# Optimization experiments

Hardware: AMD Instinct MI355X
Metric: run time of the kernel (lower is better)

## Reference

```python
import jax, jax.numpy as jnp
import numpy as np
import math

HEAD_DIM = 64
EMBED_DIM = 512
B, T = 16, 2048

def setup_inputs() -> dict:
    key = jax.random.key(0)
    k1, k2, k3 = jax.random.split(key, 3)
    x = jax.random.normal(k1, (B, T, EMBED_DIM), dtype=jnp.float32)
    # nn.Linear-style init scale
    s = 1.0 / math.sqrt(EMBED_DIM)
    Wq = jax.random.uniform(k2, (EMBED_DIM, HEAD_DIM), dtype=jnp.float32, minval=-s, maxval=s)
    bq = jax.random.uniform(k3, (HEAD_DIM,), dtype=jnp.float32, minval=-s, maxval=s)
    return {"x": x, "Wq": Wq, "bq": bq}

def reference(x, Wq, bq):
    # Faithful to source: q, k, v all come from the SAME query projection.
    q = jnp.einsum('bte,ed->btd', x, Wq) + bq  # [B,T,D]
    d_k = q.shape[-1]
    # weights[b, i, j] = q_i . q_j / sqrt(d_k)
    weights = jnp.einsum('bid,bjd->bij', q, q) / jnp.sqrt(jnp.float32(d_k))
    # NOTE: source applies softmax over dim=1 (query/row axis), not dim=-1.
    weights = jax.nn.softmax(weights, axis=1)
    attention = jnp.einsum('bij,bjd->bid', weights, q)  # v == q in source
    return attention
```

## Files before the change

### kernel.cpp

```cpp
#include <hip/hip_runtime.h>
#include <hip/hip_bf16.h>

#define BN 16
#define TN 2048
#define DN 64
#define EN 512
#define PAD 68

using f32x4  = __attribute__((ext_vector_type(4))) float;
using bf16x8 = __attribute__((ext_vector_type(8))) short;
using bf16x4 = __attribute__((ext_vector_type(4))) short;

static __device__ __forceinline__ short f2bf(float f) {
    __hip_bfloat16 h = __float2bfloat16(f);
    return __builtin_bit_cast(short, h);
}
static __device__ __forceinline__ float bf2f(short s) {
    return __bfloat162float(__builtin_bit_cast(__hip_bfloat16, s));
}

__global__ __launch_bounds__(256) void wprep_kernel(
    const float* __restrict__ Wq, short* __restrict__ WTh,
    short* __restrict__ WTl)
{
    __shared__ float wlds[64][65];
    const int tid = threadIdx.x;
    const int k0 = blockIdx.x * 64;
    #pragma unroll
    for (int it = 0; it < 16; ++it) {
        int idx = it * 256 + tid;
        int k = idx >> 6, n = idx & 63;
        wlds[k][n] = Wq[(size_t)(k0 + k) * 64 + n];
    }
    __syncthreads();
    #pragma unroll
    for (int it = 0; it < 16; ++it) {
        int idx = it * 256 + tid;
        int n = idx >> 6, k = idx & 63;
        float v = wlds[k][n];
        short h = f2bf(v);
        short l = f2bf(v - bf2f(h));
        WTh[(size_t)n * EN + k0 + k] = h;
        WTl[(size_t)n * EN + k0 + k] = l;
    }
}

__global__ __launch_bounds__(256, 2) void qproj_kernel(
    const float* __restrict__ x, const short* __restrict__ WTh,
    const short* __restrict__ WTl, const float* __restrict__ bq,
    short* __restrict__ Qb, short* __restrict__ QTb)
{
    __shared__ short xh[64 * 40];
    __shared__ short wth[64 * 40];
    __shared__ short wtl[64 * 40];
    __shared__ short tl[64][68];

    const int tid = threadIdx.x;
    const int lane = tid & 63;
    const int wv = tid >> 6;
    const int c = lane & 15;
    const int g = lane >> 4;
    const int rowbase = blockIdx.x * 64;
    const int b = rowbase >> 11;
    const int tbase = rowbase & (TN - 1);

    const int sr = tid >> 3;
    const int sc4 = tid & 7;

    float4 xa = *reinterpret_cast<const float4*>(&x[(size_t)(rowbase + sr) * EN + sc4 * 4]);
    float4 xb = *reinterpret_cast<const float4*>(&x[(size_t)(rowbase + 32 + sr) * EN + sc4 * 4]);
    bf16x4 wa = *reinterpret_cast<const bf16x4*>(&WTh[(size_t)sr * EN + sc4 * 4]);
    bf16x4 wb = *reinterpret_cast<const bf16x4*>(&WTh[(size_t)(32 + sr) * EN + sc4 * 4]);
    bf16x4 la = *reinterpret_cast<const bf16x4*>(&WTl[(size_t)sr * EN + sc4 * 4]);
    bf16x4 lb = *reinterpret_cast<const bf16x4*>(&WTl[(size_t)(32 + sr) * EN + sc4 * 4]);

    f32x4 acc[4];
    #pragma unroll
    for (int nt = 0; nt < 4; ++nt) acc[nt] = (f32x4){0.f, 0.f, 0.f, 0.f};

    for (int ks = 0; ks < EN; ks += 32) {
        __syncthreads();
        bf16x4 h0, h1;
        #pragma unroll
        for (int j = 0; j < 4; ++j) { h0[j] = f2bf(xa[j]); h1[j] = f2bf(xb[j]); }
        *reinterpret_cast<bf16x4*>(&xh[sr * 40 + sc4 * 4]) = h0;
        *reinterpret_cast<bf16x4*>(&xh[(32 + sr) * 40 + sc4 * 4]) = h1;
        *reinterpret_cast<bf16x4*>(&wth[sr * 40 + sc4 * 4]) = wa;
        *reinterpret_cast<bf16x4*>(&wth[(32 + sr) * 40 + sc4 * 4]) = wb;
        *reinterpret_cast<bf16x4*>(&wtl[sr * 40 + sc4 * 4]) = la;
        *reinterpret_cast<bf16x4*>(&wtl[(32 + sr) * 40 + sc4 * 4]) = lb;

        const int kn = (ks + 32 < EN) ? ks + 32 : ks;
        xa = *reinterpret_cast<const float4*>(&x[(size_t)(rowbase + sr) * EN + kn + sc4 * 4]);
        xb = *reinterpret_cast<const float4*>(&x[(size_t)(rowbase + 32 + sr) * EN + kn + sc4 * 4]);
        wa = *reinterpret_cast<const bf16x4*>(&WTh[(size_t)sr * EN + kn + sc4 * 4]);
        wb = *reinterpret_cast<const bf16x4*>(&WTh[(size_t)(32 + sr) * EN + kn + sc4 * 4]);
        la = *reinterpret_cast<const bf16x4*>(&WTl[(size_t)sr * EN + kn + sc4 * 4]);
        lb = *reinterpret_cast<const bf16x4*>(&WTl[(size_t)(32 + sr) * EN + kn + sc4 * 4]);
        __syncthreads();

        bf16x8 av = *reinterpret_cast<const bf16x8*>(&xh[(wv * 16 + c) * 40 + g * 8]);
        #pragma unroll
        for (int nt = 0; nt < 4; ++nt) {
            bf16x8 bh = *reinterpret_cast<const bf16x8*>(&wth[(nt * 16 + c) * 40 + g * 8]);
            bf16x8 bl = *reinterpret_cast<const bf16x8*>(&wtl[(nt * 16 + c) * 40 + g * 8]);
            acc[nt] = __builtin_amdgcn_mfma_f32_16x16x32_bf16(av, bh, acc[nt], 0, 0, 0);
            acc[nt] = __builtin_amdgcn_mfma_f32_16x16x32_bf16(av, bl, acc[nt], 0, 0, 0);
        }
    }

    __syncthreads();
    #pragma unroll
    for (int nt = 0; nt < 4; ++nt) {
        const float bias = bq[nt * 16 + c];
        #pragma unroll
        for (int r = 0; r < 4; ++r) {
            const int row = wv * 16 + g * 4 + r;
            short qb = f2bf(acc[nt][r] + bias);
            Qb[(size_t)(rowbase + row) * DN + nt * 16 + c] = qb;
            tl[nt * 16 + c][row] = qb;
        }
    }
    __syncthreads();
    #pragma unroll
    for (int it = 0; it < 4; ++it) {
        int idx = it * 256 + tid;
        int d = idx >> 4;
        int j4 = (idx & 15) * 4;
        *reinterpret_cast<short4*>(&QTb[((size_t)(b * 64 + d)) * TN + tbase + j4]) =
            *reinterpret_cast<const short4*>(&tl[d][j4]);
    }
}

__global__ __launch_bounds__(256, 4) void stats_kernel(
    const short* __restrict__ Qb, float* __restrict__ l_part)
{
    __shared__ short Qt[64 * PAD];
    const int tid = threadIdx.x;
    const int lane = tid & 63;
    const int wv = tid >> 6;
    const int c = lane & 15;
    const int g = lane >> 4;
    const int b = blockIdx.y;
    const int z = blockIdx.z;
    const int jbase = blockIdx.x * 64 + wv * 16;
    const short* Qbb = Qb + (size_t)b * TN * DN;

    bf16x8 a0 = *reinterpret_cast<const bf16x8*>(Qbb + (size_t)(jbase + c) * DN + g * 8);
    bf16x8 a1 = *reinterpret_cast<const bf16x8*>(Qbb + (size_t)(jbase + c) * DN + g * 8 + 32);

    const int srow = tid >> 2;
    const int schk = tid & 3;
    const int ilo = z * (TN / 4);

    bf16x8 v0 = *reinterpret_cast<const bf16x8*>(Qbb + (size_t)(ilo + srow) * DN + schk * 16);
    bf16x8 v1 = *reinterpret_cast<const bf16x8*>(Qbb + (size_t)(ilo + srow) * DN + schk * 16 + 8);

    float l[4] = {0.f, 0.f, 0.f, 0.f};
    for (int ii = 0; ii < TN / 4; ii += 64) {
        __syncthreads();
        *reinterpret_cast<bf16x8*>(&Qt[srow * PAD + schk * 16]) = v0;
        *reinterpret_cast<bf16x8*>(&Qt[srow * PAD + schk * 16 + 8]) = v1;
        const int in_ = ilo + ((ii + 64 < TN / 4) ? ii + 64 : ii);
        v0 = *reinterpret_cast<const bf16x8*>(Qbb + (size_t)(in_ + srow) * DN + schk * 16);
        v1 = *reinterpret_cast<const bf16x8*>(Qbb + (size_t)(in_ + srow) * DN + schk * 16 + 8);
        __syncthreads();

        #pragma unroll
        for (int it = 0; it < 4; ++it) {
            bf16x8 b0 = *reinterpret_cast<const bf16x8*>(&Qt[(it * 16 + c) * PAD + g * 8]);
            bf16x8 b1 = *reinterpret_cast<const bf16x8*>(&Qt[(it * 16 + c) * PAD + g * 8 + 32]);
            f32x4 acc = {0.f, 0.f, 0.f, 0.f};
            acc = __builtin_amdgcn_mfma_f32_16x16x32_bf16(a0, b0, acc, 0, 0, 0);
            acc = __builtin_amdgcn_mfma_f32_16x16x32_bf16(a1, b1, acc, 0, 0, 0);
            #pragma unroll
            for (int r = 0; r < 4; ++r)
                l[r] += __expf(acc[r] * 0.125f);
        }
    }
    #pragma unroll
    for (int r = 0; r < 4; ++r) {
        float v = l[r];
        v += __shfl_xor(v, 1);
        v += __shfl_xor(v, 2);
        v += __shfl_xor(v, 4);
        v += __shfl_xor(v, 8);
        l[r] = v;
    }
    if (c == 0) {
        #pragma unroll
        for (int r = 0; r < 4; ++r)
            l_part[((size_t)z * BN + b) * TN + jbase + g * 4 + r] = l[r];
    }
}

__global__ __launch_bounds__(256) void fuse_kernel(
    const short* __restrict__ QTb, const float* __restrict__ l_part,
    short* __restrict__ RT)
{
    const int idx = blockIdx.x * 256 + threadIdx.x;
    const int c8 = idx & 255;
    const int bd = idx >> 8;
    const int b = bd >> 6;
    const int j0 = c8 * 8;

    bf16x8 q = *reinterpret_cast<const bf16x8*>(&QTb[(size_t)bd * TN + j0]);
    const float* lp0 = l_part + (size_t)b * TN + j0;
    const float* lp1 = l_part + (size_t)(BN + b) * TN + j0;
    const float* lp2 = l_part + (size_t)(2 * BN + b) * TN + j0;
    const float* lp3 = l_part + (size_t)(3 * BN + b) * TN + j0;
    bf16x8 r;
    #pragma unroll
    for (int t = 0; t < 8; ++t)
        r[t] = f2bf(bf2f(q[t]) / (lp0[t] + lp1[t] + lp2[t] + lp3[t]));
    *reinterpret_cast<bf16x8*>(&RT[(size_t)bd * TN + j0]) = r;
}

__global__ __launch_bounds__(256, 2) void pv_kernel(
    const short* __restrict__ Qb, const short* __restrict__ RT,
    float* __restrict__ out0, float* __restrict__ out1)
{
    __shared__ short Qt[64 * PAD];
    __shared__ short RTt[64 * PAD];
    __shared__ short Pt[8][16 * PAD];

    const int tid = threadIdx.x;
    const int lane = tid & 63;
    const int wv = tid >> 6;
    const int c = lane & 15;
    const int g = lane >> 4;
    const int b = blockIdx.y;
    const int z = blockIdx.z;
    const int ibase = blockIdx.x * 128 + wv * 32;
    const short* Qbb = Qb + (size_t)b * TN * DN;
    const short* RTb = RT + (size_t)b * DN * TN;

    bf16x8 bi[2][2];
    #pragma unroll
    for (int ih = 0; ih < 2; ++ih) {
        const short* p = Qbb + (size_t)(ibase + ih * 16 + c) * DN + g * 8;
        bi[ih][0] = *reinterpret_cast<const bf16x8*>(p);
        bi[ih][1] = *reinterpret_cast<const bf16x8*>(p + 32);
    }

    f32x4 o[4][2];
    #pragma unroll
    for (int dt = 0; dt < 4; ++dt)
        #pragma unroll
        for (int ih = 0; ih < 2; ++ih)
            o[dt][ih] = (f32x4){0.f, 0.f, 0.f, 0.f};

    const int srow = tid >> 2;
    const int schk = tid & 3;
    const int jlo = z * (TN / 2);

    bf16x8 vq0 = *reinterpret_cast<const bf16x8*>(Qbb + (size_t)(jlo + srow) * DN + schk * 16);
    bf16x8 vq1 = *reinterpret_cast<const bf16x8*>(Qbb + (size_t)(jlo + srow) * DN + schk * 16 + 8);
    bf16x8 vt0 = *reinterpret_cast<const bf16x8*>(RTb + (size_t)srow * TN + jlo + schk * 16);
    bf16x8 vt1 = *reinterpret_cast<const bf16x8*>(RTb + (size_t)srow * TN + jlo + schk * 16 + 8);

    for (int jj = 0; jj < TN / 2; jj += 64) {
        __syncthreads();
        *reinterpret_cast<bf16x8*>(&Qt[srow * PAD + schk * 16]) = vq0;
        *reinterpret_cast<bf16x8*>(&Qt[srow * PAD + schk * 16 + 8]) = vq1;
        *reinterpret_cast<bf16x8*>(&RTt[srow * PAD + schk * 16]) = vt0;
        *reinterpret_cast<bf16x8*>(&RTt[srow * PAD + schk * 16 + 8]) = vt1;

        const int jn = jlo + ((jj + 64 < TN / 2) ? jj + 64 : jj);
        vq0 = *reinterpret_cast<const bf16x8*>(Qbb + (size_t)(jn + srow) * DN + schk * 16);
        vq1 = *reinterpret_cast<const bf16x8*>(Qbb + (size_t)(jn + srow) * DN + schk * 16 + 8);
        vt0 = *reinterpret_cast<const bf16x8*>(RTb + (size_t)srow * TN + jn + schk * 16);
        vt1 = *reinterpret_cast<const bf16x8*>(RTb + (size_t)srow * TN + jn + schk * 16 + 8);
        __syncthreads();

        bf16x8 aq[4][2];
        #pragma unroll
        for (int dt = 0; dt < 4; ++dt) {
            aq[dt][0] = *reinterpret_cast<const bf16x8*>(&RTt[(dt * 16 + c) * PAD + g * 8]);
            aq[dt][1] = *reinterpret_cast<const bf16x8*>(&RTt[(dt * 16 + c) * PAD + 32 + g * 8]);
        }

        #pragma unroll
        for (int jt = 0; jt < 4; ++jt) {
            bf16x8 a0 = *reinterpret_cast<const bf16x8*>(&Qt[(jt * 16 + c) * PAD + g * 8]);
            bf16x8 a1 = *reinterpret_cast<const bf16x8*>(&Qt[(jt * 16 + c) * PAD + g * 8 + 32]);
            #pragma unroll
            for (int ih = 0; ih < 2; ++ih) {
                f32x4 accs = {0.f, 0.f, 0.f, 0.f};
                accs = __builtin_amdgcn_mfma_f32_16x16x32_bf16(a0, bi[ih][0], accs, 0, 0, 0);
                accs = __builtin_amdgcn_mfma_f32_16x16x32_bf16(a1, bi[ih][1], accs, 0, 0, 0);
                bf16x4 pw;
                #pragma unroll
                for (int r = 0; r < 4; ++r)
                    pw[r] = f2bf(__expf(accs[r] * 0.125f));
                *reinterpret_cast<bf16x4*>(&Pt[wv * 2 + ih][c * PAD + jt * 16 + g * 4]) = pw;
            }
        }
        asm volatile("s_waitcnt lgkmcnt(0)" ::: "memory");
        __builtin_amdgcn_sched_barrier(0);

        #pragma unroll
        for (int ih = 0; ih < 2; ++ih) {
            bf16x8 p0 = *reinterpret_cast<const bf16x8*>(&Pt[wv * 2 + ih][c * PAD + g * 8]);
            bf16x8 p1 = *reinterpret_cast<const bf16x8*>(&Pt[wv * 2 + ih][c * PAD + 32 + g * 8]);
            #pragma unroll
            for (int dt = 0; dt < 4; ++dt) {
                o[dt][ih] = __builtin_amdgcn_mfma_f32_16x16x32_bf16(aq[dt][0], p0, o[dt][ih], 0, 0, 0);
                o[dt][ih] = __builtin_amdgcn_mfma_f32_16x16x32_bf16(aq[dt][1], p1, o[dt][ih], 0, 0, 0);
            }
        }
    }

    float* outb = (z ? out1 : out0) + (size_t)b * TN * DN;
    #pragma unroll
    for (int dt = 0; dt < 4; ++dt) {
        #pragma unroll
        for (int ih = 0; ih < 2; ++ih) {
            float4 v4;
            v4.x = o[dt][ih][0]; v4.y = o[dt][ih][1];
            v4.z = o[dt][ih][2]; v4.w = o[dt][ih][3];
            *reinterpret_cast<float4*>(
                &outb[(size_t)(ibase + ih * 16 + c) * DN + dt * 16 + g * 4]) = v4;
        }
    }
}

__global__ __launch_bounds__(256) void reduce_kernel(
    float* __restrict__ out, const float* __restrict__ part1)
{
    const size_t i = (size_t)blockIdx.x * 256 + threadIdx.x;
    float4 a = reinterpret_cast<float4*>(out)[i];
    float4 b = reinterpret_cast<const float4*>(part1)[i];
    a.x += b.x; a.y += b.y; a.z += b.z; a.w += b.w;
    reinterpret_cast<float4*>(out)[i] = a;
}

extern "C" void kernel_launch(void* const* d_in, const int* in_sizes, int n_in,
                              void* d_out, int out_size, void* d_ws, size_t ws_size,
                              hipStream_t stream) {
    const float* x  = (const float*)d_in[0];
    const float* Wq = (const float*)d_in[1];
    const float* bq = (const float*)d_in[2];
    float* out = (float*)d_out;

    short* Qb   = (short*)d_ws;
    short* QTb  = Qb + (size_t)BN * TN * DN;
    short* RT   = QTb + (size_t)BN * TN * DN;
    float* lpar = (float*)(RT + (size_t)BN * TN * DN);
    short* WTh  = (short*)(lpar + (size_t)4 * BN * TN);
    short* WTl  = WTh + (size_t)DN * EN;
    float* part1 = (float*)(WTl + (size_t)DN * EN);

    wprep_kernel<<<dim3(EN / 64), dim3(256), 0, stream>>>(Wq, WTh, WTl);
    qproj_kernel<<<dim3(BN * TN / 64), dim3(256), 0, stream>>>(x, WTh, WTl, bq, Qb, QTb);
    stats_kernel<<<dim3(TN / 64, BN, 4), dim3(256), 0, stream>>>(Qb, lpar);
    fuse_kernel<<<dim3(BN * DN * TN / 8 / 256), dim3(256), 0, stream>>>(QTb, lpar, RT);
    pv_kernel<<<dim3(TN / 128, BN, 2), dim3(256), 0, stream>>>(Qb, RT, out, part1);
    reduce_kernel<<<dim3(BN * TN * DN / 4 / 256), dim3(256), 0, stream>>>(out, part1);
}
```

Before: 79.22 us.

## Double-buffer LDS tiles in qproj, stats and attention kernels with one barrier

Converts the three tiled kernels from single-buffered LDS staging with two __syncthreads per iteration to ping-pong LDS buffers with a register prefetch two tiles ahead. Each iteration now needs only one lgkmcnt wait plus s_barrier. The aim is to overlap LDS stores of the next tile with MFMA work on the current tile and to halve barrier cost. In exchange LDS use doubles, which may limit occupancy in the attention kernel that also holds Pt.

Result: no change. 78.75 us, median of 2 (-0.6%).

```diff
diff --git a/kernel.cpp b/kernel.cpp
--- a/kernel.cpp
+++ b/kernel.cpp
@@ -17,6 +17,10 @@
 }
 static __device__ __forceinline__ float bf2f(short s) {
     return __bfloat162float(__builtin_bit_cast(__hip_bfloat16, s));
+}
+static __device__ __forceinline__ void bar_lds() {
+    asm volatile("s_waitcnt lgkmcnt(0)" ::: "memory");
+    __builtin_amdgcn_s_barrier();
 }
 
 __global__ __launch_bounds__(256) void wprep_kernel(
@@ -50,9 +54,9 @@
     const short* __restrict__ WTl, const float* __restrict__ bq,
     short* __restrict__ Qb, short* __restrict__ QTb)
 {
-    __shared__ short xh[64 * 40];
-    __shared__ short wth[64 * 40];
-    __shared__ short wtl[64 * 40];
+    __shared__ short xh[2 * 64 * 40];
+    __shared__ short wth[2 * 64 * 40];
+    __shared__ short wtl[2 * 64 * 40];
     __shared__ short tl[64][68];
 
     const int tid = threadIdx.x;
@@ -66,20 +70,21 @@
 
     const int sr = tid >> 3;
     const int sc4 = tid & 7;
-
-    float4 xa = *reinterpret_cast<const float4*>(&x[(size_t)(rowbase + sr) * EN + sc4 * 4]);
-    float4 xb = *reinterpret_cast<const float4*>(&x[(size_t)(rowbase + 32 + sr) * EN + sc4 * 4]);
-    bf16x4 wa = *reinterpret_cast<const bf16x4*>(&WTh[(size_t)sr * EN + sc4 * 4]);
-    bf16x4 wb = *reinterpret_cast<const bf16x4*>(&WTh[(size_t)(32 + sr) * EN + sc4 * 4]);
-    bf16x4 la = *reinterpret_cast<const bf16x4*>(&WTl[(size_t)sr * EN + sc4 * 4]);
-    bf16x4 lb = *reinterpret_cast<const bf16x4*>(&WTl[(size_t)(32 + sr) * EN + sc4 * 4]);
-
-    f32x4 acc[4];
-    #pragma unroll
-    for (int nt = 0; nt < 4; ++nt) acc[nt] = (f32x4){0.f, 0.f, 0.f, 0.f};
-
-    for (int ks = 0; ks < EN; ks += 32) {
-        __syncthreads();
+    const size_t xr0 = (size_t)(rowbase + sr) * EN + sc4 * 4;
+    const size_t xr1 = (size_t)(rowbase + 32 + sr) * EN + sc4 * 4;
+    const size_t wr0 = (size_t)sr * EN + sc4 * 4;
+    const size_t wr1 = (size_t)(32 + sr) * EN + sc4 * 4;
+
+    float4 xa, xb;
+    bf16x4 wa, wb, la, lb;
+
+    xa = *reinterpret_cast<const float4*>(&x[xr0]);
+    xb = *reinterpret_cast<const float4*>(&x[xr1]);
+    wa = *reinterpret_cast<const bf16x4*>(&WTh[wr0]);
+    wb = *reinterpret_cast<const bf16x4*>(&WTh[wr1]);
+    la = *reinterpret_cast<const bf16x4*>(&WTl[wr0]);
+    lb = *reinterpret_cast<const bf16x4*>(&WTl[wr1]);
+    {
         bf16x4 h0, h1;
         #pragma unroll
         for (int j = 0; j < 4; ++j) { h0[j] = f2bf(xa[j]); h1[j] = f2bf(xb[j]); }
@@ -89,24 +94,53 @@
         *reinterpret_cast<bf16x4*>(&wth[(32 + sr) * 40 + sc4 * 4]) = wb;
         *reinterpret_cast<bf16x4*>(&wtl[sr * 40 + sc4 * 4]) = la;
         *reinterpret_cast<bf16x4*>(&wtl[(32 + sr) * 40 + sc4 * 4]) = lb;
-
-        const int kn = (ks + 32 < EN) ? ks + 32 : ks;
-        xa = *reinterpret_cast<const float4*>(&x[(size_t)(rowbase + sr) * EN + kn + sc4 * 4]);
-        xb = *reinterpret_cast<const float4*>(&x[(size_t)(rowbase + 32 + sr) * EN + kn + sc4 * 4]);
-        wa = *reinterpret_cast<const bf16x4*>(&WTh[(size_t)sr * EN + kn + sc4 * 4]);
-        wb = *reinterpret_cast<const bf16x4*>(&WTh[(size_t)(32 + sr) * EN + kn + sc4 * 4]);
-        la = *reinterpret_cast<const bf16x4*>(&WTl[(size_t)sr * EN + kn + sc4 * 4]);
-        lb = *reinterpret_cast<const bf16x4*>(&WTl[(size_t)(32 + sr) * EN + kn + sc4 * 4]);
-        __syncthreads();
-
-        bf16x8 av = *reinterpret_cast<const bf16x8*>(&xh[(wv * 16 + c) * 40 + g * 8]);
+    }
+    xa = *reinterpret_cast<const float4*>(&x[xr0 + 32]);
+    xb = *reinterpret_cast<const float4*>(&x[xr1 + 32]);
+    wa = *reinterpret_cast<const bf16x4*>(&WTh[wr0 + 32]);
+    wb = *reinterpret_cast<const bf16x4*>(&WTh[wr1 + 32]);
+    la = *reinterpret_cast<const bf16x4*>(&WTl[wr0 + 32]);
+    lb = *reinterpret_cast<const bf16x4*>(&WTl[wr1 + 32]);
+    bar_lds();
+
+    f32x4 acc[4];
+    #pragma unroll
+    for (int nt = 0; nt < 4; ++nt) acc[nt] = (f32x4){0.f, 0.f, 0.f, 0.f};
+
+    for (int t = 0; t < 16; ++t) {
+        const int cur = t & 1;
+        const int co = cur * 2560;
+        if (t + 1 < 16) {
+            const int wo = (cur ^ 1) * 2560;
+            bf16x4 h0, h1;
+            #pragma unroll
+            for (int j = 0; j < 4; ++j) { h0[j] = f2bf(xa[j]); h1[j] = f2bf(xb[j]); }
+            *reinterpret_cast<bf16x4*>(&xh[wo + sr * 40 + sc4 * 4]) = h0;
+            *reinterpret_cast<bf16x4*>(&xh[wo + (32 + sr) * 40 + sc4 * 4]) = h1;
+            *reinterpret_cast<bf16x4*>(&wth[wo + sr * 40 + sc4 * 4]) = wa;
+            *reinterpret_cast<bf16x4*>(&wth[wo + (32 + sr) * 40 + sc4 * 4]) = wb;
+            *reinterpret_cast<bf16x4*>(&wtl[wo + sr * 40 + sc4 * 4]) = la;
+            *reinterpret_cast<bf16x4*>(&wtl[wo + (32 + sr) * 40 + sc4 * 4]) = lb;
+        }
+        if (t + 2 < 16) {
+            const int kn = (t + 2) * 32;
+            xa = *reinterpret_cast<const float4*>(&x[xr0 + kn]);
+            xb = *reinterpret_cast<const float4*>(&x[xr1 + kn]);
+            wa = *reinterpret_cast<const bf16x4*>(&WTh[wr0 + kn]);
+            wb = *reinterpret_cast<const bf16x4*>(&WTh[wr1 + kn]);
+            la = *reinterpret_cast<const bf16x4*>(&WTl[wr0 + kn]);
+            lb = *reinterpret_cast<const bf16x4*>(&WTl[wr1 + kn]);
+        }
+
+        bf16x8 av = *reinterpret_cast<const bf16x8*>(&xh[co + (wv * 16 + c) * 40 + g * 8]);
         #pragma unroll
         for (int nt = 0; nt < 4; ++nt) {
-            bf16x8 bh = *reinterpret_cast<const bf16x8*>(&wth[(nt * 16 + c) * 40 + g * 8]);
-            bf16x8 bl = *reinterpret_cast<const bf16x8*>(&wtl[(nt * 16 + c) * 40 + g * 8]);
+            bf16x8 bh = *reinterpret_cast<const bf16x8*>(&wth[co + (nt * 16 + c) * 40 + g * 8]);
+            bf16x8 bl = *reinterpret_cast<const bf16x8*>(&wtl[co + (nt * 16 + c) * 40 + g * 8]);
             acc[nt] = __builtin_amdgcn_mfma_f32_16x16x32_bf16(av, bh, acc[nt], 0, 0, 0);
             acc[nt] = __builtin_amdgcn_mfma_f32_16x16x32_bf16(av, bl, acc[nt], 0, 0, 0);
         }
+        bar_lds();
     }
 
     __syncthreads();
@@ -135,7 +169,7 @@
 __global__ __launch_bounds__(256, 4) void stats_kernel(
     const short* __restrict__ Qb, float* __restrict__ l_part)
 {
-    __shared__ short Qt[64 * PAD];
+    __shared__ short Qt[2 * 64 * PAD];
     const int tid = threadIdx.x;
     const int lane = tid & 63;
     const int wv = tid >> 6;
@@ -152,24 +186,35 @@
     const int srow = tid >> 2;
     const int schk = tid & 3;
     const int ilo = z * (TN / 4);
-
-    bf16x8 v0 = *reinterpret_cast<const bf16x8*>(Qbb + (size_t)(ilo + srow) * DN + schk * 16);
-    bf16x8 v1 = *reinterpret_cast<const bf16x8*>(Qbb + (size_t)(ilo + srow) * DN + schk * 16 + 8);
+    const int NT = (TN / 4) / 64;
+
+    bf16x8 v0, v1;
+    v0 = *reinterpret_cast<const bf16x8*>(Qbb + (size_t)(ilo + srow) * DN + schk * 16);
+    v1 = *reinterpret_cast<const bf16x8*>(Qbb + (size_t)(ilo + srow) * DN + schk * 16 + 8);
+    *reinterpret_cast<bf16x8*>(&Qt[srow * PAD + schk * 16]) = v0;
+    *reinterpret_cast<bf16x8*>(&Qt[srow * PAD + schk * 16 + 8]) = v1;
+    v0 = *reinterpret_cast<const bf16x8*>(Qbb + (size_t)(ilo + 64 + srow) * DN + schk * 16);
+    v1 = *reinterpret_cast<const bf16x8*>(Qbb + (size_t)(ilo + 64 + srow) * DN + schk * 16 + 8);
+    bar_lds();
 
     float l[4] = {0.f, 0.f, 0.f, 0.f};
-    for (int ii = 0; ii < TN / 4; ii += 64) {
-        __syncthreads();
-        *reinterpret_cast<bf16x8*>(&Qt[srow * PAD + schk * 16]) = v0;
-        *reinterpret_cast<bf16x8*>(&Qt[srow * PAD + schk * 16 + 8]) = v1;
-        const int in_ = ilo + ((ii + 64 < TN / 4) ? ii + 64 : ii);
-        v0 = *reinterpret_cast<const bf16x8*>(Qbb + (size_t)(in_ + srow) * DN + schk * 16);
-        v1 = *reinterpret_cast<const bf16x8*>(Qbb + (size_t)(in_ + srow) * DN + schk * 16 + 8);
-        __syncthreads();
-
+    for (int t = 0; t < NT; ++t) {
+        const int cur = t & 1;
+        const int co = cur * 64 * PAD;
+        if (t + 1 < NT) {
+            const int wo = (cur ^ 1) * 64 * PAD;
+            *reinterpret_cast<bf16x8*>(&Qt[wo + srow * PAD + schk * 16]) = v0;
+            *reinterpret_cast<bf16x8*>(&Qt[wo + srow * PAD + schk * 16 + 8]) = v1;
+        }
+        if (t + 2 < NT) {
+            const int in_ = ilo + (t + 2) * 64;
+            v0 = *reinterpret_cast<const bf16x8*>(Qbb + (size_t)(in_ + srow) * DN + schk * 16);
+            v1 = *reinterpret_cast<const bf16x8*>(Qbb + (size_t)(in_ + srow) * DN + schk * 16 + 8);
+        }
         #pragma unroll
         for (int it = 0; it < 4; ++it) {
-            bf16x8 b0 = *reinterpret_cast<const bf16x8*>(&Qt[(it * 16 + c) * PAD + g * 8]);
-            bf16x8 b1 = *reinterpret_cast<const bf16x8*>(&Qt[(it * 16 + c) * PAD + g * 8 + 32]);
+            bf16x8 b0 = *reinterpret_cast<const bf16x8*>(&Qt[co + (it * 16 + c) * PAD + g * 8]);
+            bf16x8 b1 = *reinterpret_cast<const bf16x8*>(&Qt[co + (it * 16 + c) * PAD + g * 8 + 32]);
             f32x4 acc = {0.f, 0.f, 0.f, 0.f};
             acc = __builtin_amdgcn_mfma_f32_16x16x32_bf16(a0, b0, acc, 0, 0, 0);
             acc = __builtin_amdgcn_mfma_f32_16x16x32_bf16(a1, b1, acc, 0, 0, 0);
@@ -177,6 +222,7 @@
             for (int r = 0; r < 4; ++r)
                 l[r] += __expf(acc[r] * 0.125f);
         }
+        bar_lds();
     }
     #pragma unroll
     for (int r = 0; r < 4; ++r) {
@@ -220,8 +266,8 @@
     const short* __restrict__ Qb, const short* __restrict__ RT,
     float* __restrict__ out0, float* __restrict__ out1)
 {
-    __shared__ short Qt[64 * PAD];
-    __shared__ short RTt[64 * PAD];
+    __shared__ short Qt[2 * 64 * PAD];
+    __shared__ short RTt[2 * 64 * PAD];
     __shared__ short Pt[8][16 * PAD];
 
     const int tid = threadIdx.x;
@@ -253,37 +299,52 @@
     const int srow = tid >> 2;
     const int schk = tid & 3;
     const int jlo = z * (TN / 2);
-
-    bf16x8 vq0 = *reinterpret_cast<const bf16x8*>(Qbb + (size_t)(jlo + srow) * DN + schk * 16);
-    bf16x8 vq1 = *reinterpret_cast<const bf16x8*>(Qbb + (size_t)(jlo + srow) * DN + schk * 16 + 8);
-    bf16x8 vt0 = *reinterpret_cast<const bf16x8*>(RTb + (size_t)srow * TN + jlo + schk * 16);
-    bf16x8 vt1 = *reinterpret_cast<const bf16x8*>(RTb + (size_t)srow * TN + jlo + schk * 16 + 8);
-
-    for (int jj = 0; jj < TN / 2; jj += 64) {
-        __syncthreads();
-        *reinterpret_cast<bf16x8*>(&Qt[srow * PAD + schk * 16]) = vq0;
-        *reinterpret_cast<bf16x8*>(&Qt[srow * PAD + schk * 16 + 8]) = vq1;
-        *reinterpret_cast<bf16x8*>(&RTt[srow * PAD + schk * 16]) = vt0;
-        *reinterpret_cast<bf16x8*>(&RTt[srow * PAD + schk * 16 + 8]) = vt1;
-
-        const int jn = jlo + ((jj + 64 < TN / 2) ? jj + 64 : jj);
-        vq0 = *reinterpret_cast<const bf16x8*>(Qbb + (size_t)(jn + srow) * DN + schk * 16);
-        vq1 = *reinterpret_cast<const bf16x8*>(Qbb + (size_t)(jn + srow) * DN + schk * 16 + 8);
-        vt0 = *reinterpret_cast<const bf16x8*>(RTb + (size_t)srow * TN + jn + schk * 16);
-        vt1 = *reinterpret_cast<const bf16x8*>(RTb + (size_t)srow * TN + jn + schk * 16 + 8);
-        __syncthreads();
+    const int NT = (TN / 2) / 64;
+
+    bf16x8 vq0, vq1, vt0, vt1;
+    vq0 = *reinterpret_cast<const bf16x8*>(Qbb + (size_t)(jlo + srow) * DN + schk * 16);
+    vq1 = *reinterpret_cast<const bf16x8*>(Qbb + (size_t)(jlo + srow) * DN + schk * 16 + 8);
+    vt0 = *reinterpret_cast<const bf16x8*>(RTb + (size_t)srow * TN + jlo + schk * 16);
+    vt1 = *reinterpret_cast<const bf16x8*>(RTb + (size_t)srow * TN + jlo + schk * 16 + 8);
+    *reinterpret_cast<bf16x8*>(&Qt[srow * PAD + schk * 16]) = vq0;
+    *reinterpret_cast<bf16x8*>(&Qt[srow * PAD + schk * 16 + 8]) = vq1;
+    *reinterpret_cast<bf16x8*>(&RTt[srow * PAD + schk * 16]) = vt0;
+    *reinterpret_cast<bf16x8*>(&RTt[srow * PAD + schk * 16 + 8]) = vt1;
+    vq0 = *reinterpret_cast<const bf16x8*>(Qbb + (size_t)(jlo + 64 + srow) * DN + schk * 16);
+    vq1 = *reinterpret_cast<const bf16x8*>(Qbb + (size_t)(jlo + 64 + srow) * DN + schk * 16 + 8);
+    vt0 = *reinterpret_cast<const bf16x8*>(RTb + (size_t)srow * TN + jlo + 64 + schk * 16);
+    vt1 = *reinterpret_cast<const bf16x8*>(RTb + (size_t)srow * TN + jlo + 64 + schk * 16 + 8);
+    bar_lds();
+
+    for (int t = 0; t < NT; ++t) {
+        const int cur = t & 1;
+        const int co = cur * 64 * PAD;
+        if (t + 1 < NT) {
+            const int wo = (cur ^ 1) * 64 * PAD;
+            *reinterpret_cast<bf16x8*>(&Qt[wo + srow * PAD + schk * 16]) = vq0;
+            *reinterpret_cast<bf16x8*>(&Qt[wo + srow * PAD + schk * 16 + 8]) = vq1;
+            *reinterpret_cast<bf16x8*>(&RTt[wo + srow * PAD + schk * 16]) = vt0;
+            *reinterpret_cast<bf16x8*>(&RTt[wo + srow * PAD + schk * 16 + 8]) = vt1;
+        }
+        if (t + 2 < NT) {
+            const int jn = jlo + (t + 2) * 64;
+            vq0 = *reinterpret_cast<const bf16x8*>(Qbb + (size_t)(jn + srow) * DN + schk * 16);
+            vq1 = *reinterpret_cast<const bf16x8*>(Qbb + (size_t)(jn + srow) * DN + schk * 16 + 8);
+            vt0 = *reinterpret_cast<const bf16x8*>(RTb + (size_t)srow * TN + jn + schk * 16);
+            vt1 = *reinterpret_cast<const bf16x8*>(RTb + (size_t)srow * TN + jn + schk * 16 + 8);
+        }
 
         bf16x8 aq[4][2];
         #pragma unroll
         for (int dt = 0; dt < 4; ++dt) {
-            aq[dt][0] = *reinterpret_cast<const bf16x8*>(&RTt[(dt * 16 + c) * PAD + g * 8]);
-            aq[dt][1] = *reinterpret_cast<const bf16x8*>(&RTt[(dt * 16 + c) * PAD + 32 + g * 8]);
+            aq[dt][0] = *reinterpret_cast<const bf16x8*>(&RTt[co + (dt * 16 + c) * PAD + g * 8]);
+            aq[dt][1] = *reinterpret_cast<const bf16x8*>(&RTt[co + (dt * 16 + c) * PAD + 32 + g * 8]);
         }
 
         #pragma unroll
         for (int jt = 0; jt < 4; ++jt) {
-            bf16x8 a0 = *reinterpret_cast<const bf16x8*>(&Qt[(jt * 16 + c) * PAD + g * 8]);
-            bf16x8 a1 = *reinterpret_cast<const bf16x8*>(&Qt[(jt * 16 + c) * PAD + g * 8 + 32]);
+            bf16x8 a0 = *reinterpret_cast<const bf16x8*>(&Qt[co + (jt * 16 + c) * PAD + g * 8]);
+            bf16x8 a1 = *reinterpret_cast<const bf16x8*>(&Qt[co + (jt * 16 + c) * PAD + g * 8 + 32]);
             #pragma unroll
             for (int ih = 0; ih < 2; ++ih) {
                 f32x4 accs = {0.f, 0.f, 0.f, 0.f};
@@ -309,6 +370,7 @@
                 o[dt][ih] = __builtin_amdgcn_mfma_f32_16x16x32_bf16(aq[dt][1], p1, o[dt][ih], 0, 0, 0);
             }
         }
+        bar_lds();
     }
 
     float* outb = (z ? out1 : out0) + (size_t)b * TN * DN;
```
